# Kernel optimization log

Measured on AMD Instinct MI355X. Metric: run time of the kernel, lower is better.

## Reference

```python
import jax, jax.numpy as jnp
import numpy as np

B, H, S, D = 1, 16, 4096, 64

def setup_inputs() -> dict:
    key = jax.random.key(0)
    kq, kk, kv = jax.random.split(key, 3)
    q = jax.random.normal(kq, (B, H, S, D), dtype=jnp.float32)
    k = jax.random.normal(kk, (B, H, S, D), dtype=jnp.float32)
    v = jax.random.normal(kv, (B, H, S, D), dtype=jnp.float32)
    # causal mask, broadcastable over batch and heads: True = attend
    mask = jnp.tril(jnp.ones((S, S), dtype=bool))[None, None, :, :]
    return {"q": q, "k": k, "v": v, "mask": mask}


def reference(q, k, v, mask):
    # Chunked attention in the original is mathematically identical to full
    # attention: each query-chunk softmaxes over ALL keys. Vectorized form:
    dim_head = q.shape[-1]
    scale = 1.0 / jnp.sqrt(jnp.asarray(dim_head, dtype=q.dtype))
    scores = jnp.einsum("bhqd,bhkd->bhqk", q, k) * scale  # [B,H,S,S]
    scores = jnp.where(mask, scores, -jnp.inf)
    attn = jax.nn.softmax(scores, axis=-1)
    attn = jnp.nan_to_num(attn, nan=0.0)  # rows with all keys masked -> 0
    return jnp.einsum("bhqk,bhkd->bhqd", attn, v)
```

## Files before the change

### kernel.cpp

```cpp
#include <hip/hip_runtime.h>
#include <hip/hip_bf16.h>
#include <math.h>


typedef __bf16 bf16;
typedef __bf16 bf16x8 __attribute__((ext_vector_type(8)));
typedef float f32x16 __attribute__((ext_vector_type(16)));

#define NH 16
#define SEQ 4096
#define DH 64
#define QB 128
#define WQ 32
#define KB 64
#define LOG2E 1.44269504088896340736f

static __device__ __forceinline__ void mfma32(f32x16& c, bf16x8 a, bf16x8 b) {
  asm("v_mfma_f32_32x32x16_bf16 %0, %1, %2, %0" : "+v"(c) : "v"(a), "v"(b));
}
static __device__ __forceinline__ float exp2a(float x) {
  float r; asm("v_exp_f32 %0, %1" : "=v"(r) : "v"(x)); return r;
}
static __device__ __forceinline__ unsigned pk(float lo, float hi) {
  unsigned r; asm("v_cvt_pk_bf16_f32 %0, %1, %2" : "=v"(r) : "v"(lo), "v"(hi)); return r;
}
static __device__ __forceinline__ void swap32(unsigned& a, unsigned& b) {
  asm("v_permlane32_swap_b32 %0, %1" : "+v"(a), "+v"(b));
}

union AFrag { unsigned u[4]; bf16x8 v; };

__global__ __launch_bounds__(256, 2)
void fa_fwd(const float* __restrict__ Q, const float* __restrict__ K,
            const float* __restrict__ V, float* __restrict__ O) {
  __shared__ bf16 Ksh[KB * DH];
  __shared__ bf16 Vt[DH * KB];

  const int bid  = blockIdx.x;
  const int head = bid & (NH - 1);
  const int qblk = (SEQ / QB - 1) - (bid >> 4);
  const int qb   = qblk * QB;

  const int tid = threadIdx.x;
  const int w   = tid >> 6;
  const int l   = tid & 63;
  const int lc  = l & 31;
  const int hi  = l >> 5;
  const int qw  = qb + w * WQ;
  const int qv  = qw + lc;

  const float* Qh = Q + (size_t)head * SEQ * DH;
  const float* Kh = K + (size_t)head * SEQ * DH;
  const float* Vh = V + (size_t)head * SEQ * DH;

  bf16x8 qf[4];
  {
    const float* qp = Qh + (size_t)qv * DH + hi * 8;
    const float sc = 0.125f * LOG2E;
#pragma unroll
    for (int ch = 0; ch < 4; ++ch) {
      float4 x = *(const float4*)(qp + ch * 16);
      float4 y = *(const float4*)(qp + ch * 16 + 4);
      bf16x8 f;
      f[0]=(bf16)(x.x*sc); f[1]=(bf16)(x.y*sc); f[2]=(bf16)(x.z*sc); f[3]=(bf16)(x.w*sc);
      f[4]=(bf16)(y.x*sc); f[5]=(bf16)(y.y*sc); f[6]=(bf16)(y.z*sc); f[7]=(bf16)(y.w*sc);
      qf[ch] = f;
    }
  }

  f32x16 o0 = {}, o1 = {};
  float m = -INFINITY, ls = 0.f;

  const int skr = tid >> 2,        skc = (tid & 3) << 4;
  const int svr = (tid >> 3) << 1, svc = (tid & 7) << 3;

  const int nt = (qb + QB) / KB;
  for (int t = 0; t < nt; ++t) {
    const int kb = t * KB;
    __syncthreads();
    {
      const float* p = Kh + (size_t)(kb + skr) * DH + skc;
      float4 a0 = ((const float4*)p)[0], a1 = ((const float4*)p)[1];
      float4 a2 = ((const float4*)p)[2], a3 = ((const float4*)p)[3];
      bf16x8 f0, f1;
      f0[0]=(bf16)a0.x; f0[1]=(bf16)a0.y; f0[2]=(bf16)a0.z; f0[3]=(bf16)a0.w;
      f0[4]=(bf16)a1.x; f0[5]=(bf16)a1.y; f0[6]=(bf16)a1.z; f0[7]=(bf16)a1.w;
      f1[0]=(bf16)a2.x; f1[1]=(bf16)a2.y; f1[2]=(bf16)a2.z; f1[3]=(bf16)a2.w;
      f1[4]=(bf16)a3.x; f1[5]=(bf16)a3.y; f1[6]=(bf16)a3.z; f1[7]=(bf16)a3.w;
      const int base = skr * 128 + skc * 2, sw = (skr & 7) << 4;
      *(bf16x8*)((char*)Ksh + (base ^ sw))        = f0;
      *(bf16x8*)((char*)Ksh + ((base + 16) ^ sw)) = f1;
    }
    {
      const float* p0 = Vh + (size_t)(kb + svr) * DH + svc;
      const float* p1 = p0 + DH;
      float4 a0 = ((const float4*)p0)[0], a1 = ((const float4*)p0)[1];
      float4 b0 = ((const float4*)p1)[0], b1 = ((const float4*)p1)[1];
      float va[8] = {a0.x,a0.y,a0.z,a0.w,a1.x,a1.y,a1.z,a1.w};
      float vb[8] = {b0.x,b0.y,b0.z,b0.w,b1.x,b1.y,b1.z,b1.w};
#pragma unroll
      for (int i = 0; i < 8; ++i) {
        const int c = svc + i;
        *(unsigned*)((char*)Vt + ((c * 128 + svr * 2) ^ ((c & 7) << 4))) = pk(va[i], vb[i]);
      }
    }
    __syncthreads();
    if (kb > qw + WQ - 1) continue;

    f32x16 st0 = {}, st1 = {};
#pragma unroll
    for (int ch = 0; ch < 4; ++ch) {
      const int boff = ch * 32 + hi * 16, sw = (lc & 7) << 4;
      bf16x8 k0 = *(const bf16x8*)((const char*)Ksh + ((lc * 128 + boff) ^ sw));
      bf16x8 k1 = *(const bf16x8*)((const char*)Ksh + (((lc + 32) * 128 + boff) ^ sw));
      mfma32(st0, k0, qf[ch]);
      mfma32(st1, k1, qf[ch]);
    }

    if (kb + KB - 1 > qw) {
#pragma unroll
      for (int r = 0; r < 16; ++r) {
        const int k0 = kb + ((r & 3) + 8 * (r >> 2) + 4 * hi);
        if (k0 > qv)      st0[r] = -INFINITY;
        if (k0 + 32 > qv) st1[r] = -INFINITY;
      }
    }

    float acc[8];
#pragma unroll
    for (int i = 0; i < 8; ++i)
      acc[i] = fmaxf(fmaxf(st0[i], st0[i + 8]), fmaxf(st1[i], st1[i + 8]));
    acc[0]=fmaxf(acc[0],acc[4]); acc[1]=fmaxf(acc[1],acc[5]);
    acc[2]=fmaxf(acc[2],acc[6]); acc[3]=fmaxf(acc[3],acc[7]);
    acc[0]=fmaxf(acc[0],acc[2]); acc[1]=fmaxf(acc[1],acc[3]);
    float mx = fmaxf(acc[0], acc[1]);
    mx = fmaxf(mx, __shfl_xor(mx, 32));

    if (__any(mx > m + 8.0f)) {
      const float mn = fmaxf(m, mx);
      const float al = exp2a(m - mn);
      m = mn;
      ls *= al;
#pragma unroll
      for (int r = 0; r < 16; ++r) {
        const float aq = __shfl(al, (r & 3) + 8 * (r >> 2) + 4 * hi);
        o0[r] *= aq; o1[r] *= aq;
      }
    }

    float rs = 0.f;
    unsigned wA[4][4];
#pragma unroll
    for (int half = 0; half < 4; ++half) {
      float p[8];
#pragma unroll
      for (int j = 0; j < 8; ++j) {
        const float s = (half < 2) ? st0[(half & 1) * 8 + j] : st1[(half & 1) * 8 + j];
        p[j] = exp2a(s - m);
      }
      rs += ((p[0]+p[1])+(p[2]+p[3])) + ((p[4]+p[5])+(p[6]+p[7]));
      unsigned u0 = pk(p[0],p[1]), u1 = pk(p[2],p[3]);
      unsigned u2 = pk(p[4],p[5]), u3 = pk(p[6],p[7]);
      swap32(u0, u2); swap32(u1, u3);
      wA[half][0]=u0; wA[half][1]=u1; wA[half][2]=u2; wA[half][3]=u3;
    }
    rs += __shfl_xor(rs, 32);
    ls += rs;

#pragma unroll
    for (int ks = 0; ks < 4; ++ks) {
      AFrag af; af.u[0]=wA[ks][0]; af.u[1]=wA[ks][1]; af.u[2]=wA[ks][2]; af.u[3]=wA[ks][3];
      const int koff = ks * 32 + hi * 16, sw = (lc & 7) << 4;
      bf16x8 v0 = *(const bf16x8*)((const char*)Vt + ((lc * 128 + koff) ^ sw));
      bf16x8 v1 = *(const bf16x8*)((const char*)Vt + (((lc + 32) * 128 + koff) ^ sw));
      mfma32(o0, af.v, v0);
      mfma32(o1, af.v, v1);
    }
  }

  const float inv = 1.0f / ls;
  float* Ob = O + (size_t)(head * SEQ + qw) * DH;
#pragma unroll
  for (int r = 0; r < 16; ++r) {
    const int row = (r & 3) + 8 * (r >> 2) + 4 * hi;
    const float iq = __shfl(inv, row);
    Ob[(size_t)row * DH + lc]      = o0[r] * iq;
    Ob[(size_t)row * DH + 32 + lc] = o1[r] * iq;
  }
}

extern "C" void kernel_launch(void* const* d_in, const int* in_sizes, int n_in,
                              void* d_out, int out_size, void* d_ws, size_t ws_size,
                              hipStream_t stream) {
  const float* q = (const float*)d_in[0];
  const float* k = (const float*)d_in[1];
  const float* v = (const float*)d_in[2];
  float* out = (float*)d_out;
  dim3 grid(NH * (SEQ / QB));
  dim3 block(256);
  fa_fwd<<<grid, block, 0, stream>>>(q, k, v, out);
}
```

Measured before the change: 249.1 us.

## Double-buffer K/V tiles with register prefetch and 128-key tiles

```diff
diff --git a/kernel.cpp b/kernel.cpp
--- a/kernel.cpp
+++ b/kernel.cpp
@@ -12,7 +12,7 @@
 #define DH 64
 #define QB 128
 #define WQ 32
-#define KB 64
+#define KB 128
 #define LOG2E 1.44269504088896340736f
 
 static __device__ __forceinline__ void mfma32(f32x16& c, bf16x8 a, bf16x8 b) {
@@ -29,12 +29,19 @@
 }
 
 union AFrag { unsigned u[4]; bf16x8 v; };
+
+static __device__ __forceinline__ bf16x8 cvt8(float4 a, float4 b) {
+  bf16x8 f;
+  f[0]=(bf16)a.x; f[1]=(bf16)a.y; f[2]=(bf16)a.z; f[3]=(bf16)a.w;
+  f[4]=(bf16)b.x; f[5]=(bf16)b.y; f[6]=(bf16)b.z; f[7]=(bf16)b.w;
+  return f;
+}
 
 __global__ __launch_bounds__(256, 2)
 void fa_fwd(const float* __restrict__ Q, const float* __restrict__ K,
             const float* __restrict__ V, float* __restrict__ O) {
-  __shared__ bf16 Ksh[KB * DH];
-  __shared__ bf16 Vt[DH * KB];
+  __shared__ bf16 Ksh[2][KB * DH];
+  __shared__ bf16 Vts[2][DH * KB];
 
   const int bid  = blockIdx.x;
   const int head = bid & (NH - 1);
@@ -71,111 +78,142 @@
   f32x16 o0 = {}, o1 = {};
   float m = -INFINITY, ls = 0.f;
 
-  const int skr = tid >> 2,        skc = (tid & 3) << 4;
-  const int svr = (tid >> 3) << 1, svc = (tid & 7) << 3;
-
-  const int nt = (qb + QB) / KB;
+  const int kr = tid >> 1, kc = (tid & 1) * 32;
+  const int dg = tid & 7,  kp2 = tid >> 3;
+
+  float4 kreg[8], vreg[8];
+  const int nt = qblk + 1;
+
+  {
+    const float* p = Kh + (size_t)kr * DH + kc;
+#pragma unroll
+    for (int i = 0; i < 8; ++i) kreg[i] = ((const float4*)p)[i];
+#pragma unroll
+    for (int u = 0; u < 2; ++u) {
+      const float* pv = Vh + (size_t)(2 * (kp2 + 32 * u)) * DH + dg * 8;
+      vreg[u*4+0] = ((const float4*)pv)[0];
+      vreg[u*4+1] = ((const float4*)pv)[1];
+      vreg[u*4+2] = ((const float4*)(pv + DH))[0];
+      vreg[u*4+3] = ((const float4*)(pv + DH))[1];
+    }
+  }
+
   for (int t = 0; t < nt; ++t) {
     const int kb = t * KB;
+    const int b  = t & 1;
+
+    {
+      const int Sk = (((kr & 7) ^ ((kr >> 3) & 7)) << 4);
+#pragma unroll
+      for (int q = 0; q < 4; ++q)
+        *(bf16x8*)((char*)Ksh[b] + kr * 128 + ((kc * 2 + q * 16) ^ Sk)) =
+            cvt8(kreg[2*q], kreg[2*q+1]);
+      const int xbase = (kp2 * 4) ^ (dg << 4);
+#pragma unroll
+      for (int u = 0; u < 2; ++u) {
+        const int xb = xbase + u * 128;
+#pragma unroll
+        for (int i = 0; i < 8; ++i) {
+          const float lo = vreg[u*4 + (i >> 2)    ][i & 3];
+          const float hv = vreg[u*4 + (i >> 2) + 2][i & 3];
+          *(unsigned*)((char*)Vts[b] + (dg * 8 + i) * 256 + (xb ^ (i << 4))) =
+              pk(lo, hv);
+        }
+      }
+    }
     __syncthreads();
-    {
-      const float* p = Kh + (size_t)(kb + skr) * DH + skc;
-      float4 a0 = ((const float4*)p)[0], a1 = ((const float4*)p)[1];
-      float4 a2 = ((const float4*)p)[2], a3 = ((const float4*)p)[3];
-      bf16x8 f0, f1;
-      f0[0]=(bf16)a0.x; f0[1]=(bf16)a0.y; f0[2]=(bf16)a0.z; f0[3]=(bf16)a0.w;
-      f0[4]=(bf16)a1.x; f0[5]=(bf16)a1.y; f0[6]=(bf16)a1.z; f0[7]=(bf16)a1.w;
-      f1[0]=(bf16)a2.x; f1[1]=(bf16)a2.y; f1[2]=(bf16)a2.z; f1[3]=(bf16)a2.w;
-      f1[4]=(bf16)a3.x; f1[5]=(bf16)a3.y; f1[6]=(bf16)a3.z; f1[7]=(bf16)a3.w;
-      const int base = skr * 128 + skc * 2, sw = (skr & 7) << 4;
-      *(bf16x8*)((char*)Ksh + (base ^ sw))        = f0;
-      *(bf16x8*)((char*)Ksh + ((base + 16) ^ sw)) = f1;
-    }
-    {
-      const float* p0 = Vh + (size_t)(kb + svr) * DH + svc;
-      const float* p1 = p0 + DH;
-      float4 a0 = ((const float4*)p0)[0], a1 = ((const float4*)p0)[1];
-      float4 b0 = ((const float4*)p1)[0], b1 = ((const float4*)p1)[1];
-      float va[8] = {a0.x,a0.y,a0.z,a0.w,a1.x,a1.y,a1.z,a1.w};
-      float vb[8] = {b0.x,b0.y,b0.z,b0.w,b1.x,b1.y,b1.z,b1.w};
-#pragma unroll
-      for (int i = 0; i < 8; ++i) {
-        const int c = svc + i;
-        *(unsigned*)((char*)Vt + ((c * 128 + svr * 2) ^ ((c & 7) << 4))) = pk(va[i], vb[i]);
-      }
-    }
-    __syncthreads();
-    if (kb > qw + WQ - 1) continue;
-
-    f32x16 st0 = {}, st1 = {};
-#pragma unroll
-    for (int ch = 0; ch < 4; ++ch) {
-      const int boff = ch * 32 + hi * 16, sw = (lc & 7) << 4;
-      bf16x8 k0 = *(const bf16x8*)((const char*)Ksh + ((lc * 128 + boff) ^ sw));
-      bf16x8 k1 = *(const bf16x8*)((const char*)Ksh + (((lc + 32) * 128 + boff) ^ sw));
-      mfma32(st0, k0, qf[ch]);
-      mfma32(st1, k1, qf[ch]);
-    }
-
-    if (kb + KB - 1 > qw) {
-#pragma unroll
-      for (int r = 0; r < 16; ++r) {
-        const int k0 = kb + ((r & 3) + 8 * (r >> 2) + 4 * hi);
-        if (k0 > qv)      st0[r] = -INFINITY;
-        if (k0 + 32 > qv) st1[r] = -INFINITY;
-      }
-    }
-
-    float acc[8];
-#pragma unroll
-    for (int i = 0; i < 8; ++i)
-      acc[i] = fmaxf(fmaxf(st0[i], st0[i + 8]), fmaxf(st1[i], st1[i + 8]));
-    acc[0]=fmaxf(acc[0],acc[4]); acc[1]=fmaxf(acc[1],acc[5]);
-    acc[2]=fmaxf(acc[2],acc[6]); acc[3]=fmaxf(acc[3],acc[7]);
-    acc[0]=fmaxf(acc[0],acc[2]); acc[1]=fmaxf(acc[1],acc[3]);
-    float mx = fmaxf(acc[0], acc[1]);
-    mx = fmaxf(mx, __shfl_xor(mx, 32));
-
-    if (__any(mx > m + 8.0f)) {
-      const float mn = fmaxf(m, mx);
-      const float al = exp2a(m - mn);
-      m = mn;
-      ls *= al;
-#pragma unroll
-      for (int r = 0; r < 16; ++r) {
-        const float aq = __shfl(al, (r & 3) + 8 * (r >> 2) + 4 * hi);
-        o0[r] *= aq; o1[r] *= aq;
-      }
-    }
-
-    float rs = 0.f;
-    unsigned wA[4][4];
-#pragma unroll
-    for (int half = 0; half < 4; ++half) {
-      float p[8];
-#pragma unroll
-      for (int j = 0; j < 8; ++j) {
-        const float s = (half < 2) ? st0[(half & 1) * 8 + j] : st1[(half & 1) * 8 + j];
-        p[j] = exp2a(s - m);
-      }
-      rs += ((p[0]+p[1])+(p[2]+p[3])) + ((p[4]+p[5])+(p[6]+p[7]));
-      unsigned u0 = pk(p[0],p[1]), u1 = pk(p[2],p[3]);
-      unsigned u2 = pk(p[4],p[5]), u3 = pk(p[6],p[7]);
-      swap32(u0, u2); swap32(u1, u3);
-      wA[half][0]=u0; wA[half][1]=u1; wA[half][2]=u2; wA[half][3]=u3;
-    }
-    rs += __shfl_xor(rs, 32);
-    ls += rs;
-
-#pragma unroll
-    for (int ks = 0; ks < 4; ++ks) {
-      AFrag af; af.u[0]=wA[ks][0]; af.u[1]=wA[ks][1]; af.u[2]=wA[ks][2]; af.u[3]=wA[ks][3];
-      const int koff = ks * 32 + hi * 16, sw = (lc & 7) << 4;
-      bf16x8 v0 = *(const bf16x8*)((const char*)Vt + ((lc * 128 + koff) ^ sw));
-      bf16x8 v1 = *(const bf16x8*)((const char*)Vt + (((lc + 32) * 128 + koff) ^ sw));
-      mfma32(o0, af.v, v0);
-      mfma32(o1, af.v, v1);
-    }
+
+    if (t + 1 < nt) {
+      const int kn = kb + KB;
+      const float* p = Kh + (size_t)(kn + kr) * DH + kc;
+#pragma unroll
+      for (int i = 0; i < 8; ++i) kreg[i] = ((const float4*)p)[i];
+#pragma unroll
+      for (int u = 0; u < 2; ++u) {
+        const float* pv = Vh + (size_t)(kn + 2 * (kp2 + 32 * u)) * DH + dg * 8;
+        vreg[u*4+0] = ((const float4*)pv)[0];
+        vreg[u*4+1] = ((const float4*)pv)[1];
+        vreg[u*4+2] = ((const float4*)(pv + DH))[0];
+        vreg[u*4+3] = ((const float4*)(pv + DH))[1];
+      }
+    }
+
+#pragma unroll
+    for (int hb = 0; hb < 2; ++hb) {
+      if (kb + hb * 64 > qw + 31) continue;
+
+      f32x16 st0 = {}, st1 = {};
+#pragma unroll
+      for (int kt = 0; kt < 2; ++kt) {
+        const int row = hb * 64 + kt * 32;
+        const int Sr  = (((lc & 7) ^ ((kt * 4 + (lc >> 3)) & 7)) << 4);
+        f32x16& st = kt ? st1 : st0;
+#pragma unroll
+        for (int ch = 0; ch < 4; ++ch) {
+          const bf16x8 kf = *(const bf16x8*)((const char*)Ksh[b] +
+              (row + lc) * 128 + ((ch * 32 + hi * 16) ^ Sr));
+          mfma32(st, kf, qf[ch]);
+        }
+      }
+
+      if (kb + hb * 64 + 63 > qw) {
+#pragma unroll
+        for (int r = 0; r < 16; ++r) {
+          const int kg = kb + hb * 64 + ((r & 3) + 8 * (r >> 2) + 4 * hi);
+          if (kg > qv)      st0[r] = -INFINITY;
+          if (kg + 32 > qv) st1[r] = -INFINITY;
+        }
+      }
+
+      float acc[8];
+#pragma unroll
+      for (int i = 0; i < 8; ++i)
+        acc[i] = fmaxf(fmaxf(st0[i], st0[i + 8]), fmaxf(st1[i], st1[i + 8]));
+      acc[0]=fmaxf(acc[0],acc[4]); acc[1]=fmaxf(acc[1],acc[5]);
+      acc[2]=fmaxf(acc[2],acc[6]); acc[3]=fmaxf(acc[3],acc[7]);
+      acc[0]=fmaxf(acc[0],acc[2]); acc[1]=fmaxf(acc[1],acc[3]);
+      float mx = fmaxf(acc[0], acc[1]);
+      mx = fmaxf(mx, __shfl_xor(mx, 32));
+
+      if (__any(mx > m + 8.0f)) {
+        const float mn = fmaxf(m, mx);
+        const float al = exp2a(m - mn);
+        m = mn;
+        ls *= al;
+#pragma unroll
+        for (int r = 0; r < 16; ++r) {
+          const float aq = __shfl(al, (r & 3) + 8 * (r >> 2) + 4 * hi);
+          o0[r] *= aq; o1[r] *= aq;
+        }
+      }
+
+      float rs = 0.f;
+#pragma unroll
+      for (int ks = 0; ks < 4; ++ks) {
+        const f32x16& st = (ks < 2) ? st0 : st1;
+        float p[8];
+#pragma unroll
+        for (int j = 0; j < 8; ++j) p[j] = exp2a(st[(ks & 1) * 8 + j] - m);
+        rs += ((p[0]+p[1])+(p[2]+p[3])) + ((p[4]+p[5])+(p[6]+p[7]));
+        unsigned u0 = pk(p[0],p[1]), u1 = pk(p[2],p[3]);
+        unsigned u2 = pk(p[4],p[5]), u3 = pk(p[6],p[7]);
+        swap32(u0, u2); swap32(u1, u3);
+        AFrag af; af.u[0]=u0; af.u[1]=u1; af.u[2]=u2; af.u[3]=u3;
+        const int koff = hb * 128 + ks * 32 + hi * 16;
+        const int S0 = (((lc & 7) ^ ((lc >> 3) & 7)) << 4);
+        const int S1 = (((lc & 7) ^ (((lc >> 3) + 4) & 7)) << 4);
+        bf16x8 v0 = *(const bf16x8*)((const char*)Vts[b] +
+            lc * 256 + (koff ^ S0));
+        bf16x8 v1 = *(const bf16x8*)((const char*)Vts[b] +
+            (lc + 32) * 256 + (koff ^ S1));
+        mfma32(o0, af.v, v0);
+        mfma32(o1, af.v, v1);
+      }
+      rs += __shfl_xor(rs, 32);
+      ls += rs;
+    }
+
+    if (t + 1 < nt) __syncthreads();
   }
 
   const float inv = 1.0f / ls;
```

Result: faster. 221.9 us (-10.9%).
